# Performance work log

Hardware: AMD Instinct MI355X
Metric: run time of the kernel (lower is better)

## Reference

```python
import jax, jax.numpy as jnp
import numpy as np
from jax import lax

REPR, ACT, HID = 256, 2, 512
BN_EPS = 1e-5


def setup_inputs() -> dict:
    key = jax.random.key(0)
    ks = jax.random.split(key, 12)
    B, H, W, Tm1 = 512, 64, 64, 16
    d_in = REPR + ACT
    s = lambda k, shape, scale: jax.random.normal(k, shape, dtype=jnp.float32) * scale
    return {
        "init_state": jax.random.normal(ks[0], (B, 2, H, W), dtype=jnp.float32),
        "actions": jax.random.normal(ks[1], (B, Tm1, ACT), dtype=jnp.float32),
        "conv_w": s(ks[2], (16, 2, 3, 3), (1.0 / np.sqrt(2 * 9))),
        "bn_gamma": jnp.ones((16,), jnp.float32),
        "bn_beta": jnp.zeros((16,), jnp.float32),
        "enc_fc_w": s(ks[3], (REPR, 16), (1.0 / np.sqrt(16))),
        "enc_fc_b": s(ks[4], (REPR,), 0.01),
        "gru_w_ih": s(ks[5], (3 * HID, d_in), (1.0 / np.sqrt(HID))),
        "gru_w_hh": s(ks[6], (3 * HID, HID), (1.0 / np.sqrt(HID))),
        "gru_b_ih": s(ks[7], (3 * HID,), (1.0 / np.sqrt(HID))),
        "gru_b_hh": s(ks[8], (3 * HID,), (1.0 / np.sqrt(HID))),
        "pred_fc_w": s(ks[9], (REPR, HID), (1.0 / np.sqrt(HID))),
        "pred_fc_b": s(ks[10], (REPR,), 0.01),
    }


def _encoder(x, conv_w, bn_gamma, bn_beta, enc_fc_w, enc_fc_b):
    # Conv2d(2->16, 3x3, stride 1, pad 1, no bias), NCHW
    y = lax.conv_general_dilated(x, conv_w, (1, 1), "SAME",
                                 dimension_numbers=("NCHW", "OIHW", "NCHW"))
    # BatchNorm2d in training mode: batch statistics over (N, H, W)
    mean = jnp.mean(y, axis=(0, 2, 3), keepdims=True)
    var = jnp.var(y, axis=(0, 2, 3), keepdims=True)
    y = (y - mean) * lax.rsqrt(var + BN_EPS)
    y = y * bn_gamma[None, :, None, None] + bn_beta[None, :, None, None]
    y = jax.nn.relu(y)
    # MaxPool2d(2, 2)
    y = lax.reduce_window(y, -jnp.inf, lax.max, (1, 1, 2, 2), (1, 1, 2, 2), "VALID")
    # AdaptiveAvgPool2d((1,1)) + flatten
    y = jnp.mean(y, axis=(2, 3))  # (B, 16)
    return y @ enc_fc_w.T + enc_fc_b  # (B, repr_dim)


def reference(init_state, actions, conv_w, bn_gamma, bn_beta, enc_fc_w, enc_fc_b,
              gru_w_ih, gru_w_hh, gru_b_ih, gru_b_hh, pred_fc_w, pred_fc_b):
    B = init_state.shape[0]
    s0 = _encoder(init_state, conv_w, bn_gamma, bn_beta, enc_fc_w, enc_fc_b)  # (B, R)

    def step(carry, u_t):
        s_prev, h = carry
        x = jnp.concatenate([s_prev, u_t], axis=-1)          # (B, R+A)
        gx = x @ gru_w_ih.T + gru_b_ih                        # (B, 3H)
        gh = h @ gru_w_hh.T + gru_b_hh                        # (B, 3H)
        gx_r, gx_z, gx_n = jnp.split(gx, 3, axis=-1)
        gh_r, gh_z, gh_n = jnp.split(gh, 3, axis=-1)
        r = jax.nn.sigmoid(gx_r + gh_r)
        z = jax.nn.sigmoid(gx_z + gh_z)
        n = jnp.tanh(gx_n + r * gh_n)
        h_new = (1.0 - z) * n + z * h
        s_pred = jax.nn.relu(h_new @ pred_fc_w.T + pred_fc_b)  # (B, R)
        return (s_pred, h_new), s_pred

    h0 = jnp.zeros((B, HID), dtype=s0.dtype)
    u_seq = jnp.transpose(actions, (1, 0, 2))  # (T-1, B, A)
    _, preds = lax.scan(step, (s0, h0), u_seq)  # preds: (T-1, B, R)
    pred_encs = jnp.concatenate([s0[None], preds], axis=0)  # (T, B, R)
    return jnp.transpose(pred_encs, (1, 0, 2))  # (B, T, R)
```

## Files before the change

kernel.cpp:

```cpp
#include <hip/hip_runtime.h>
#include <hip/hip_bf16.h>
#include <math.h>

#define TM1 16
#define TT 17

typedef __attribute__((ext_vector_type(8))) __bf16 bf16x8;
typedef __attribute__((ext_vector_type(4))) float f32x4;

#define OFF_BSTATS 0
#define OFF_STATS  65536
#define OFF_POOLED 65568
#define OFF_BCOL   98336
#define OFF_SPB    104480
#define OFF_PWB    170016
#define OFF_WIHB   235552
#define OFF_WHHB   432160
#define OFF_HB     825376
#define OFF_RP     1087520

#define IMG_STRIDE 67
#define SLAB_ROWS 18
#define IMG_CI (SLAB_ROWS * IMG_STRIDE)

__device__ __forceinline__ void stage_slab_bf16(__hip_bfloat16* __restrict__ imgp,
                                                const float* __restrict__ xb, int slab,
                                                int tid) {
  for (int i = tid; i < 2 * SLAB_ROWS * 66; i += 256) {
    const int ci = i / (SLAB_ROWS * 66);
    const int rem = i - ci * (SLAB_ROWS * 66);
    const int lr = rem / 66, c = rem - lr * 66;
    const int gr = slab * 16 - 1 + lr;
    float v = 0.0f;
    if (gr >= 0 && gr < 64 && c >= 1 && c <= 64) v = xb[ci * 4096 + gr * 64 + (c - 1)];
    imgp[ci * IMG_CI + lr * IMG_STRIDE + c] = __float2bfloat16(v);
  }
}

__device__ __forceinline__ void make_k_offsets(int hi, int* off, int* val) {
#pragma unroll
  for (int j = 0; j < 8; ++j) {
    const int k = hi * 8 + j;
    if (k < 18) {
      const int ci = k / 9, r9 = k - ci * 9;
      const int dy = r9 / 3, dx = r9 - dy * 3;
      off[j] = ci * IMG_CI + dy * IMG_STRIDE + dx;
      val[j] = 1;
    } else {
      off[j] = 0;
      val[j] = 0;
    }
  }
}

__device__ __forceinline__ bf16x8 make_conv_bfrag(const float* __restrict__ cw,
                                                  int l15, int hi) {
  __hip_bfloat16 btmp[8];
#pragma unroll
  for (int j = 0; j < 8; ++j) {
    const int k = hi * 8 + j;
    btmp[j] = __float2bfloat16((k < 18) ? cw[l15 * 18 + k] : 0.0f);
  }
  return *(bf16x8*)btmp;
}

__device__ __forceinline__ bf16x8 make_conv_afrag(const __hip_bfloat16* __restrict__ imgp,
                                                  int yloc, int x0, int l15,
                                                  const int* off, const int* val) {
  const int base = yloc * IMG_STRIDE + x0 + l15;
  const __hip_bfloat16 z = __float2bfloat16(0.0f);
  __hip_bfloat16 atmp[8];
#pragma unroll
  for (int j = 0; j < 8; ++j) atmp[j] = val[j] ? imgp[base + off[j]] : z;
  return *(bf16x8*)atmp;
}

__global__ __launch_bounds__(256) void enc_stats_prep(
    const float* __restrict__ x, const float* __restrict__ cw,
    float* __restrict__ bstats,
    const float* __restrict__ wih, const float* __restrict__ whh,
    const float* __restrict__ pw,
    const float* __restrict__ bih, const float* __restrict__ bhh,
    __hip_bfloat16* __restrict__ wihb, __hip_bfloat16* __restrict__ whhb,
    __hip_bfloat16* __restrict__ pwb, float* __restrict__ bcol) {
  {
    const int n1 = 1536 * 256, n2 = 1536 * 512, n3 = 256 * 512, n4 = 512 * 12;
    int i = blockIdx.x * 256 + threadIdx.x;
    int st = gridDim.x * 256;
    for (int j = i; j < n1 + n2 + n3 + n4; j += st) {
      if (j < n1) {
        int r = j >> 8, c = j & 255;
        wihb[j] = __float2bfloat16(wih[r * 258 + c]);
      } else if (j < n1 + n2) {
        int k = j - n1;
        whhb[k] = __float2bfloat16(whh[k]);
      } else if (j < n1 + n2 + n3) {
        int k = j - n1 - n2;
        pwb[k] = __float2bfloat16(pw[k]);
      } else {
        int k = j - n1 - n2 - n3;
        int col = k / 12, e = k - col * 12;
        float v = 0.0f;
        switch (e) {
          case 0: v = bih[col] + bhh[col]; break;
          case 1: v = bih[512 + col] + bhh[512 + col]; break;
          case 2: v = bih[1024 + col]; break;
          case 3: v = bhh[1024 + col]; break;
          case 4: v = wih[col * 258 + 256]; break;
          case 5: v = wih[col * 258 + 257]; break;
          case 6: v = wih[(512 + col) * 258 + 256]; break;
          case 7: v = wih[(512 + col) * 258 + 257]; break;
          case 8: v = wih[(1024 + col) * 258 + 256]; break;
          case 9: v = wih[(1024 + col) * 258 + 257]; break;
          default: v = 0.0f; break;
        }
        bcol[k] = v;
      }
    }
  }

  __shared__ __hip_bfloat16 imgp[2 * IMG_CI];
  __shared__ float redS[4][16], redQ[4][16];
  const int tid = threadIdx.x;
  const int b = blockIdx.x >> 2, slab = blockIdx.x & 3;
  const int wv = tid >> 6, lane = tid & 63;
  const int l15 = lane & 15, hi = lane >> 4;
  stage_slab_bf16(imgp, x + b * 8192, slab, tid);

  int off[8], val[8];
  make_k_offsets(hi, off, val);
  const bf16x8 bfrag = make_conv_bfrag(cw, l15, hi);
  __syncthreads();

  float sacc = 0.0f, qacc = 0.0f;
  const f32x4 zero4 = {0.f, 0.f, 0.f, 0.f};
#pragma unroll
  for (int tp = 0; tp < 8; ++tp) {
    const int tpi = wv * 8 + tp;
    const int y0 = (tpi >> 2) * 2, x0 = (tpi & 3) * 16;
    bf16x8 a0 = make_conv_afrag(imgp, y0, x0, l15, off, val);
    bf16x8 a1 = make_conv_afrag(imgp, y0 + 1, x0, l15, off, val);
    f32x4 c0 = __builtin_amdgcn_mfma_f32_16x16x32_bf16(a0, bfrag, zero4, 0, 0, 0);
    f32x4 c1 = __builtin_amdgcn_mfma_f32_16x16x32_bf16(a1, bfrag, zero4, 0, 0, 0);
#pragma unroll
    for (int i = 0; i < 4; ++i) {
      sacc += c0[i] + c1[i];
      qacc = fmaf(c0[i], c0[i], qacc);
      qacc = fmaf(c1[i], c1[i], qacc);
    }
  }
  sacc += __shfl_down(sacc, 16); sacc += __shfl_down(sacc, 32);
  qacc += __shfl_down(qacc, 16); qacc += __shfl_down(qacc, 32);
  if (lane < 16) { redS[wv][l15] = sacc; redQ[wv][l15] = qacc; }
  __syncthreads();
  if (tid < 16)
    bstats[tid * 2048 + blockIdx.x] =
        redS[0][tid] + redS[1][tid] + redS[2][tid] + redS[3][tid];
  else if (tid < 32) {
    int c = tid - 16;
    bstats[tid * 2048 + blockIdx.x] =
        redQ[0][c] + redQ[1][c] + redQ[2][c] + redQ[3][c];
  }
}

__global__ __launch_bounds__(256) void reduce_stats_k(const float* __restrict__ bstats,
                                                      float* __restrict__ stats) {
  __shared__ float acc[4];
  const int c = blockIdx.x, tid = threadIdx.x;
  const float4 v4 = *(const float4*)(bstats + c * 2048 + tid * 8);
  const float4 w4 = *(const float4*)(bstats + c * 2048 + tid * 8 + 4);
  float v = v4.x + v4.y + v4.z + v4.w + w4.x + w4.y + w4.z + w4.w;
#pragma unroll
  for (int off = 32; off >= 1; off >>= 1) v += __shfl_down(v, off);
  if ((tid & 63) == 0) acc[tid >> 6] = v;
  __syncthreads();
  if (tid == 0) stats[c] = acc[0] + acc[1] + acc[2] + acc[3];
}

__global__ __launch_bounds__(256) void enc_pool(const float* __restrict__ x,
                                                const float* __restrict__ cw,
                                                const float* __restrict__ stats,
                                                const float* __restrict__ gamma,
                                                const float* __restrict__ beta,
                                                float* __restrict__ pooledG) {
  __shared__ __hip_bfloat16 imgp[2 * IMG_CI];
  __shared__ float red[4][16];
  __shared__ float statsL[32];
  const int tid = threadIdx.x;
  const int b = blockIdx.x >> 2, slab = blockIdx.x & 3;
  const int wv = tid >> 6, lane = tid & 63;
  const int l15 = lane & 15, hi = lane >> 4;
  stage_slab_bf16(imgp, x + b * 8192, slab, tid);
  if (tid < 32) statsL[tid] = stats[tid];

  int off[8], val[8];
  make_k_offsets(hi, off, val);
  const bf16x8 bfrag = make_conv_bfrag(cw, l15, hi);
  __syncthreads();

  const float invN = 1.0f / (512.0f * 4096.0f);
  const float m = statsL[l15] * invN;
  const float var = statsL[16 + l15] * invN - m * m;
  const float isd = rsqrtf(var + 1e-5f);
  const float scv = gamma[l15] * isd;
  const float shv = beta[l15] - m * scv;

  float psum = 0.0f;
  const f32x4 zero4 = {0.f, 0.f, 0.f, 0.f};
#pragma unroll
  for (int tp = 0; tp < 8; ++tp) {
    const int tpi = wv * 8 + tp;
    const int y0 = (tpi >> 2) * 2, x0 = (tpi & 3) * 16;
    bf16x8 a0 = make_conv_afrag(imgp, y0, x0, l15, off, val);
    bf16x8 a1 = make_conv_afrag(imgp, y0 + 1, x0, l15, off, val);
    f32x4 c0 = __builtin_amdgcn_mfma_f32_16x16x32_bf16(a0, bfrag, zero4, 0, 0, 0);
    f32x4 c1 = __builtin_amdgcn_mfma_f32_16x16x32_bf16(a1, bfrag, zero4, 0, 0, 0);
#pragma unroll
    for (int p = 0; p < 2; ++p) {
      const float v00 = fmaxf(fmaf(c0[2 * p + 0], scv, shv), 0.0f);
      const float v01 = fmaxf(fmaf(c0[2 * p + 1], scv, shv), 0.0f);
      const float v10 = fmaxf(fmaf(c1[2 * p + 0], scv, shv), 0.0f);
      const float v11 = fmaxf(fmaf(c1[2 * p + 1], scv, shv), 0.0f);
      psum += fmaxf(fmaxf(v00, v01), fmaxf(v10, v11));
    }
  }
  psum += __shfl_down(psum, 16);
  psum += __shfl_down(psum, 32);
  if (lane < 16) red[wv][l15] = psum;
  __syncthreads();
  if (tid < 16)
    pooledG[blockIdx.x * 16 + tid] = red[0][tid] + red[1][tid] + red[2][tid] + red[3][tid];
}

__global__ __launch_bounds__(384) void gru_v3(
    const __hip_bfloat16* __restrict__ hb_in,
    __hip_bfloat16* __restrict__ hb_out,
    const float* __restrict__ rp_in,
    float* __restrict__ rp_out,
    const __hip_bfloat16* __restrict__ wihb,
    const __hip_bfloat16* __restrict__ whhb,
    const __hip_bfloat16* __restrict__ pwb,
    const float* __restrict__ pb,
    const float* __restrict__ bcol,
    const float* __restrict__ actions,
    const float* __restrict__ pooledG, const float* __restrict__ fcw,
    const float* __restrict__ fcb,
    float* __restrict__ out,
    int t) {
  __shared__ __hip_bfloat16 hF[16 * 64 * 8];
  __shared__ __hip_bfloat16 sL[8 * 64 * 8];
  __shared__ __hip_bfloat16 hS[2 * 64 * 8];
  __shared__ float accL[4][4][256];
  const int tid = threadIdx.x;
  const int w = tid / 64, lane = tid & 63;
  const int l15 = lane & 15, hi = lane >> 4;
  const int cg = blockIdx.x >> 5, band = blockIdx.x & 31;
  const int row0 = band * 16;

  if (t > 0) {
    for (int i = tid; i < 1024; i += 384) {
      int kk = i >> 6, ln = i & 63;
      *(bf16x8*)(hF + i * 8) =
          *(const bf16x8*)(hb_in + (row0 + (ln & 15)) * 512 + kk * 32 + (ln >> 4) * 8);
    }
    for (int i = tid; i < 1024; i += 384) {
      const int row = i >> 6, c4 = (i & 63) * 4;
      float4 a = *(const float4*)(pb + c4);
#pragma unroll
      for (int s = 0; s < 8; ++s) {
        const float4 p = *(const float4*)(rp_in + ((size_t)(s * 512 + row0 + row)) * 256 + c4);
        a.x += p.x; a.y += p.y; a.z += p.z; a.w += p.w;
      }
      a.x = fmaxf(a.x, 0.f); a.y = fmaxf(a.y, 0.f);
      a.z = fmaxf(a.z, 0.f); a.w = fmaxf(a.w, 0.f);
      const float av[4] = {a.x, a.y, a.z, a.w};
#pragma unroll
      for (int j = 0; j < 4; ++j) {
        const int c = c4 + j;
        sL[((c >> 5) * 64 + row + 16 * ((c & 31) >> 3)) * 8 + (c & 7)] =
            __float2bfloat16(av[j]);
      }
      if (cg == 0) *(float4*)(out + ((size_t)(row0 + row) * TT + t) * 256 + c4) = a;
    }
  } else {
    float* avgF = &accL[0][0][0];
    if (tid < 256) {
      const int r = tid >> 4, k = tid & 15;
      const int img = row0 + r;
      const float v = pooledG[(img * 4 + 0) * 16 + k] + pooledG[(img * 4 + 1) * 16 + k] +
                      pooledG[(img * 4 + 2) * 16 + k] + pooledG[(img * 4 + 3) * 16 + k];
      avgF[r * 16 + k] = v * (1.0f / 1024.0f);
    }
    __syncthreads();
    for (int i = tid; i < 4096; i += 384) {
      const int r = i >> 8, col = i & 255;
      float v = fcb[col];
#pragma unroll
      for (int k = 0; k < 16; ++k) v = fmaf(avgF[r * 16 + k], fcw[col * 16 + k], v);
      sL[((col >> 5) * 64 + r + 16 * ((col & 31) >> 3)) * 8 + (col & 7)] =
          __float2bfloat16(v);
      if (cg == 0) out[((size_t)(row0 + r) * TT + 0) * 256 + col] = v;
    }
  }
  __syncthreads();

#pragma unroll
  for (int jj = 0; jj < 2; ++jj) {
    const int job = 2 * w + jj;
    const int g = job >> 2, ct4 = job & 3;
    const int jb = cg * 64 + ct4 * 16 + l15;
    f32x4 accS = {0.f, 0.f, 0.f, 0.f}, accH = accS;
    {
      const __hip_bfloat16* B = wihb + (size_t)(g * 512 + jb) * 256 + hi * 8;
#pragma unroll
      for (int kk = 0; kk < 8; ++kk) {
        bf16x8 a = *(const bf16x8*)(sL + (kk * 64 + lane) * 8);
        accS = __builtin_amdgcn_mfma_f32_16x16x32_bf16(a, *(const bf16x8*)(B + kk * 32),
                                                       accS, 0, 0, 0);
      }
    }
    if (t > 0) {
      const __hip_bfloat16* B = whhb + (size_t)(g * 512 + jb) * 512 + hi * 8;
#pragma unroll
      for (int kk = 0; kk < 16; ++kk) {
        bf16x8 a = *(const bf16x8*)(hF + (kk * 64 + lane) * 8);
        accH = __builtin_amdgcn_mfma_f32_16x16x32_bf16(a, *(const bf16x8*)(B + kk * 32),
                                                       accH, 0, 0, 0);
      }
    }
    if (g < 2) {
#pragma unroll
      for (int i = 0; i < 4; ++i)
        accL[g][ct4][(hi * 4 + i) * 16 + l15] = accS[i] + accH[i];
    } else {
#pragma unroll
      for (int i = 0; i < 4; ++i) {
        accL[2][ct4][(hi * 4 + i) * 16 + l15] = accS[i];
        accL[3][ct4][(hi * 4 + i) * 16 + l15] = accH[i];
      }
    }
  }
  __syncthreads();

  if (w < 4) {
    f32x4 vR = *(const f32x4*)&accL[0][w][lane * 4];
    f32x4 vZ = *(const f32x4*)&accL[1][w][lane * 4];
    f32x4 vXN = *(const f32x4*)&accL[2][w][lane * 4];
    f32x4 vHN = *(const f32x4*)&accL[3][w][lane * 4];
    const int r = lane >> 2;
    const int row = row0 + r;
    const float u0 = actions[row * 32 + t * 2 + 0];
    const float u1 = actions[row * 32 + t * 2 + 1];
#pragma unroll
    for (int j = 0; j < 4; ++j) {
      const int c = (lane & 3) * 4 + j;
      const int kloc = w * 16 + c;
      const int col = cg * 64 + kloc;
      const float4 b0 = *(const float4*)(bcol + col * 12);
      const float4 b1 = *(const float4*)(bcol + col * 12 + 4);
      const float4 b2 = *(const float4*)(bcol + col * 12 + 8);
      const float gr = vR[j] + b0.x + u0 * b1.x + u1 * b1.y;
      const float gz = vZ[j] + b0.y + u0 * b1.z + u1 * b1.w;
      const float gxn = vXN[j] + b0.z + u0 * b2.x + u1 * b2.y;
      const float ghn = vHN[j] + b0.w;
      const float rg = 1.0f / (1.0f + __expf(-gr));
      const float zg = 1.0f / (1.0f + __expf(-gz));
      float xn = gxn + rg * ghn;
      xn = fminf(fmaxf(xn, -15.0f), 15.0f);
      const float e = __expf(2.0f * xn);
      const float ng = (e - 1.0f) / (e + 1.0f);
      const float hp = (t > 0) ? (float)hb_in[row * 512 + col] : 0.0f;
      const float hnv = (1.0f - zg) * ng + zg * hp;
      const __hip_bfloat16 hb = __float2bfloat16(hnv);
      hb_out[row * 512 + col] = hb;
      hS[((kloc >> 5) * 64 + r + 16 * ((kloc & 31) >> 3)) * 8 + (kloc & 7)] = hb;
    }
  }
  __syncthreads();

  if (t < TM1 - 1) {
    for (int ct = w; ct < 16; ct += 6) {
      const int pc = ct * 16 + l15;
      const __hip_bfloat16* bp = pwb + (size_t)pc * 512 + cg * 64 + hi * 8;
      f32x4 acc = {0.f, 0.f, 0.f, 0.f};
      acc = __builtin_amdgcn_mfma_f32_16x16x32_bf16(
          *(const bf16x8*)(hS + (0 * 64 + lane) * 8), *(const bf16x8*)(bp), acc, 0, 0, 0);
      acc = __builtin_amdgcn_mfma_f32_16x16x32_bf16(
          *(const bf16x8*)(hS + (1 * 64 + lane) * 8), *(const bf16x8*)(bp + 32), acc, 0, 0, 0);
#pragma unroll
      for (int i = 0; i < 4; ++i)
        rp_out[((size_t)(cg * 512 + row0 + hi * 4 + i)) * 256 + pc] = acc[i];
    }
  }
}

__global__ __launch_bounds__(256) void pred_v2(
    const __hip_bfloat16* __restrict__ hb,
    const __hip_bfloat16* __restrict__ pwb,
    const float* __restrict__ pb,
    float* __restrict__ out,
    __hip_bfloat16* __restrict__ spb,
    int slot) {
  __shared__ float accL[4][256];
  const int tid = threadIdx.x;
  const int w = tid >> 6, lane = tid & 63;
  const int l15 = lane & 15, hi = lane >> 4;
  const int pcg = blockIdx.x, band = blockIdx.y;
  const int row0 = band * 16, pc0 = pcg * 16;
  f32x4 acc = {0.f, 0.f, 0.f, 0.f};
  const __hip_bfloat16* A = hb + (row0 + l15) * 512 + w * 128 + hi * 8;
  const __hip_bfloat16* B = pwb + (pc0 + l15) * 512 + w * 128 + hi * 8;
#pragma unroll
  for (int kk = 0; kk < 4; ++kk)
    acc = __builtin_amdgcn_mfma_f32_16x16x32_bf16(*(const bf16x8*)(A + kk * 32),
                                                  *(const bf16x8*)(B + kk * 32),
                                                  acc, 0, 0, 0);
#pragma unroll
  for (int i = 0; i < 4; ++i) accL[w][(hi * 4 + i) * 16 + l15] = acc[i];
  __syncthreads();
  if (w == 0) {
    f32x4 p0 = *(const f32x4*)&accL[0][lane * 4];
    f32x4 p1 = *(const f32x4*)&accL[1][lane * 4];
    f32x4 p2 = *(const f32x4*)&accL[2][lane * 4];
    f32x4 p3 = *(const f32x4*)&accL[3][lane * 4];
    const int r = lane >> 2;
    const int row = row0 + r;
    float4 ov;
    float* po = &ov.x;
#pragma unroll
    for (int j = 0; j < 4; ++j) {
      const int c = (lane & 3) * 4 + j;
      const int col = pc0 + c;
      float v = p0[j] + p1[j] + p2[j] + p3[j] + pb[col];
      v = fmaxf(v, 0.0f);
      po[j] = v;
      spb[row * 256 + col] = __float2bfloat16(v);
    }
    *(float4*)(out + ((size_t)row * TT + slot) * 256 + pc0 + (lane & 3) * 4) = ov;
  }
}

extern "C" void kernel_launch(void* const* d_in, const int* in_sizes, int n_in,
                              void* d_out, int out_size, void* d_ws, size_t ws_size,
                              hipStream_t stream) {
  const float* x       = (const float*)d_in[0];
  const float* actions = (const float*)d_in[1];
  const float* cw      = (const float*)d_in[2];
  const float* gamma   = (const float*)d_in[3];
  const float* beta    = (const float*)d_in[4];
  const float* fcw     = (const float*)d_in[5];
  const float* fcb     = (const float*)d_in[6];
  const float* wih     = (const float*)d_in[7];
  const float* whh     = (const float*)d_in[8];
  const float* bih     = (const float*)d_in[9];
  const float* bhh     = (const float*)d_in[10];
  const float* pw      = (const float*)d_in[11];
  const float* pb      = (const float*)d_in[12];
  float* out = (float*)d_out;
  float* ws  = (float*)d_ws;

  float* bstats  = ws + OFF_BSTATS;
  float* stats   = ws + OFF_STATS;
  float* pooledG = ws + OFF_POOLED;
  float* bcol    = ws + OFF_BCOL;
  __hip_bfloat16* spb  = (__hip_bfloat16*)(ws + OFF_SPB);
  __hip_bfloat16* pwb  = (__hip_bfloat16*)(ws + OFF_PWB);
  __hip_bfloat16* wihb = (__hip_bfloat16*)(ws + OFF_WIHB);
  __hip_bfloat16* whhb = (__hip_bfloat16*)(ws + OFF_WHHB);
  __hip_bfloat16* hb0  = (__hip_bfloat16*)(ws + OFF_HB);
  __hip_bfloat16* hb1  = hb0 + 512 * 512;
  float* rp0 = ws + OFF_RP;
  float* rp1 = rp0 + 8 * 512 * 256;

  enc_stats_prep<<<dim3(2048), dim3(256), 0, stream>>>(x, cw, bstats, wih, whh, pw,
                                                       bih, bhh, wihb, whhb, pwb, bcol);
  reduce_stats_k<<<dim3(32), dim3(256), 0, stream>>>(bstats, stats);
  enc_pool<<<dim3(2048), dim3(256), 0, stream>>>(x, cw, stats, gamma, beta, pooledG);
  for (int t = 0; t < TM1; ++t) {
    __hip_bfloat16* hbi = (t & 1) ? hb1 : hb0;
    __hip_bfloat16* hbo = (t & 1) ? hb0 : hb1;
    float* rpi = (t & 1) ? rp1 : rp0;
    float* rpo = (t & 1) ? rp0 : rp1;
    gru_v3<<<dim3(256), dim3(384), 0, stream>>>(
        hbi, hbo, rpi, rpo, wihb, whhb, pwb, pb, bcol, actions,
        pooledG, fcw, fcb, out, t);
  }
  pred_v2<<<dim3(16, 32), dim3(256), 0, stream>>>(hb0, pwb, pb, out, spb, 16);
}
```

Before: 306.5 us.

## Split GRU step over 512 blocks with bf16 prediction partials and direct h loads

The per-step GRU kernel now covers 32 hidden columns per block instead of 64, so the grid doubles to 512 blocks and each wave handles a single gate/column job. The partial prediction sums move from fp32 to bf16 and split across 16 column groups, which halves the bytes per partial but doubles how many are summed. The recurrent h operand is read straight from global memory rather than staged in shared memory, removing a staging loop and shrinking LDS use. Risks are lower precision from bf16 partial sums and more redundant reads of the input-side activation and weights across the extra blocks.

New measurement: 414.4 us. +35.2%, slower.

```diff
diff --git a/kernel.cpp b/kernel.cpp
--- a/kernel.cpp
+++ b/kernel.cpp
@@ -6,6 +6,7 @@
 #define TT 17
 
 typedef __attribute__((ext_vector_type(8))) __bf16 bf16x8;
+typedef __attribute__((ext_vector_type(4))) __bf16 bf16x4;
 typedef __attribute__((ext_vector_type(4))) float f32x4;
 
 #define OFF_BSTATS 0
@@ -232,11 +233,11 @@
     pooledG[blockIdx.x * 16 + tid] = red[0][tid] + red[1][tid] + red[2][tid] + red[3][tid];
 }
 
-__global__ __launch_bounds__(384) void gru_v3(
+__global__ __launch_bounds__(384) void gru_v5(
     const __hip_bfloat16* __restrict__ hb_in,
     __hip_bfloat16* __restrict__ hb_out,
-    const float* __restrict__ rp_in,
-    float* __restrict__ rp_out,
+    const __hip_bfloat16* __restrict__ rp_in,
+    __hip_bfloat16* __restrict__ rp_out,
     const __hip_bfloat16* __restrict__ wihb,
     const __hip_bfloat16* __restrict__ whhb,
     const __hip_bfloat16* __restrict__ pwb,
@@ -247,10 +248,9 @@
     const float* __restrict__ fcb,
     float* __restrict__ out,
     int t) {
-  __shared__ __hip_bfloat16 hF[16 * 64 * 8];
   __shared__ __hip_bfloat16 sL[8 * 64 * 8];
-  __shared__ __hip_bfloat16 hS[2 * 64 * 8];
-  __shared__ float accL[4][4][256];
+  __shared__ __hip_bfloat16 hS[64 * 8];
+  __shared__ float accL[4][2][256];
   const int tid = threadIdx.x;
   const int w = tid / 64, lane = tid & 63;
   const int l15 = lane & 15, hi = lane >> 4;
@@ -259,28 +259,29 @@
 
   if (t > 0) {
     for (int i = tid; i < 1024; i += 384) {
-      int kk = i >> 6, ln = i & 63;
-      *(bf16x8*)(hF + i * 8) =
-          *(const bf16x8*)(hb_in + (row0 + (ln & 15)) * 512 + kk * 32 + (ln >> 4) * 8);
-    }
-    for (int i = tid; i < 1024; i += 384) {
       const int row = i >> 6, c4 = (i & 63) * 4;
-      float4 a = *(const float4*)(pb + c4);
-#pragma unroll
-      for (int s = 0; s < 8; ++s) {
-        const float4 p = *(const float4*)(rp_in + ((size_t)(s * 512 + row0 + row)) * 256 + c4);
-        a.x += p.x; a.y += p.y; a.z += p.z; a.w += p.w;
-      }
-      a.x = fmaxf(a.x, 0.f); a.y = fmaxf(a.y, 0.f);
-      a.z = fmaxf(a.z, 0.f); a.w = fmaxf(a.w, 0.f);
-      const float av[4] = {a.x, a.y, a.z, a.w};
+      float a[4];
+      {
+        const float4 pb4 = *(const float4*)(pb + c4);
+        a[0] = pb4.x; a[1] = pb4.y; a[2] = pb4.z; a[3] = pb4.w;
+      }
+#pragma unroll
+      for (int s = 0; s < 16; ++s) {
+        const bf16x4 p = *(const bf16x4*)(rp_in + ((size_t)(s * 512 + row0 + row)) * 256 + c4);
+#pragma unroll
+        for (int j = 0; j < 4; ++j) a[j] += (float)p[j];
+      }
+      float4 ov;
+      ov.x = fmaxf(a[0], 0.f); ov.y = fmaxf(a[1], 0.f);
+      ov.z = fmaxf(a[2], 0.f); ov.w = fmaxf(a[3], 0.f);
+      const float av[4] = {ov.x, ov.y, ov.z, ov.w};
 #pragma unroll
       for (int j = 0; j < 4; ++j) {
         const int c = c4 + j;
         sL[((c >> 5) * 64 + row + 16 * ((c & 31) >> 3)) * 8 + (c & 7)] =
             __float2bfloat16(av[j]);
       }
-      if (cg == 0) *(float4*)(out + ((size_t)(row0 + row) * TT + t) * 256 + c4) = a;
+      if (cg == 0) *(float4*)(out + ((size_t)(row0 + row) * TT + t) * 256 + c4) = ov;
     }
   } else {
     float* avgF = &accL[0][0][0];
@@ -301,14 +302,13 @@
           __float2bfloat16(v);
       if (cg == 0) out[((size_t)(row0 + r) * TT + 0) * 256 + col] = v;
     }
-  }
-  __syncthreads();
-
-#pragma unroll
-  for (int jj = 0; jj < 2; ++jj) {
-    const int job = 2 * w + jj;
-    const int g = job >> 2, ct4 = job & 3;
-    const int jb = cg * 64 + ct4 * 16 + l15;
+    __syncthreads();
+  }
+  __syncthreads();
+
+  {
+    const int g = w >> 1, ct2 = w & 1;
+    const int jb = cg * 32 + ct2 * 16 + l15;
     f32x4 accS = {0.f, 0.f, 0.f, 0.f}, accH = accS;
     {
       const __hip_bfloat16* B = wihb + (size_t)(g * 512 + jb) * 256 + hi * 8;
@@ -320,10 +320,11 @@
       }
     }
     if (t > 0) {
+      const __hip_bfloat16* A = hb_in + (row0 + l15) * 512 + hi * 8;
       const __hip_bfloat16* B = whhb + (size_t)(g * 512 + jb) * 512 + hi * 8;
 #pragma unroll
       for (int kk = 0; kk < 16; ++kk) {
-        bf16x8 a = *(const bf16x8*)(hF + (kk * 64 + lane) * 8);
+        bf16x8 a = *(const bf16x8*)(A + kk * 32);
         accH = __builtin_amdgcn_mfma_f32_16x16x32_bf16(a, *(const bf16x8*)(B + kk * 32),
                                                        accH, 0, 0, 0);
       }
@@ -331,18 +332,18 @@
     if (g < 2) {
 #pragma unroll
       for (int i = 0; i < 4; ++i)
-        accL[g][ct4][(hi * 4 + i) * 16 + l15] = accS[i] + accH[i];
+        accL[g][ct2][(hi * 4 + i) * 16 + l15] = accS[i] + accH[i];
     } else {
 #pragma unroll
       for (int i = 0; i < 4; ++i) {
-        accL[2][ct4][(hi * 4 + i) * 16 + l15] = accS[i];
-        accL[3][ct4][(hi * 4 + i) * 16 + l15] = accH[i];
-      }
-    }
-  }
-  __syncthreads();
-
-  if (w < 4) {
+        accL[2][ct2][(hi * 4 + i) * 16 + l15] = accS[i];
+        accL[3][ct2][(hi * 4 + i) * 16 + l15] = accH[i];
+      }
+    }
+  }
+  __syncthreads();
+
+  if (w < 2) {
     f32x4 vR = *(const f32x4*)&accL[0][w][lane * 4];
     f32x4 vZ = *(const f32x4*)&accL[1][w][lane * 4];
     f32x4 vXN = *(const f32x4*)&accL[2][w][lane * 4];
@@ -355,7 +356,7 @@
     for (int j = 0; j < 4; ++j) {
       const int c = (lane & 3) * 4 + j;
       const int kloc = w * 16 + c;
-      const int col = cg * 64 + kloc;
+      const int col = cg * 32 + kloc;
       const float4 b0 = *(const float4*)(bcol + col * 12);
       const float4 b1 = *(const float4*)(bcol + col * 12 + 4);
       const float4 b2 = *(const float4*)(bcol + col * 12 + 8);
@@ -373,23 +374,22 @@
       const float hnv = (1.0f - zg) * ng + zg * hp;
       const __hip_bfloat16 hb = __float2bfloat16(hnv);
       hb_out[row * 512 + col] = hb;
-      hS[((kloc >> 5) * 64 + r + 16 * ((kloc & 31) >> 3)) * 8 + (kloc & 7)] = hb;
+      hS[(r + 16 * (kloc >> 3)) * 8 + (kloc & 7)] = hb;
     }
   }
   __syncthreads();
 
   if (t < TM1 - 1) {
+    const bf16x8 afrag = *(const bf16x8*)(hS + lane * 8);
     for (int ct = w; ct < 16; ct += 6) {
       const int pc = ct * 16 + l15;
-      const __hip_bfloat16* bp = pwb + (size_t)pc * 512 + cg * 64 + hi * 8;
+      const __hip_bfloat16* bp = pwb + (size_t)pc * 512 + cg * 32 + hi * 8;
       f32x4 acc = {0.f, 0.f, 0.f, 0.f};
-      acc = __builtin_amdgcn_mfma_f32_16x16x32_bf16(
-          *(const bf16x8*)(hS + (0 * 64 + lane) * 8), *(const bf16x8*)(bp), acc, 0, 0, 0);
-      acc = __builtin_amdgcn_mfma_f32_16x16x32_bf16(
-          *(const bf16x8*)(hS + (1 * 64 + lane) * 8), *(const bf16x8*)(bp + 32), acc, 0, 0, 0);
+      acc = __builtin_amdgcn_mfma_f32_16x16x32_bf16(afrag, *(const bf16x8*)bp, acc, 0, 0, 0);
 #pragma unroll
       for (int i = 0; i < 4; ++i)
-        rp_out[((size_t)(cg * 512 + row0 + hi * 4 + i)) * 256 + pc] = acc[i];
+        rp_out[((size_t)(cg * 512 + row0 + hi * 4 + i)) * 256 + pc] =
+            __float2bfloat16(acc[i]);
     }
   }
 }
@@ -469,8 +469,8 @@
   __hip_bfloat16* whhb = (__hip_bfloat16*)(ws + OFF_WHHB);
   __hip_bfloat16* hb0  = (__hip_bfloat16*)(ws + OFF_HB);
   __hip_bfloat16* hb1  = hb0 + 512 * 512;
-  float* rp0 = ws + OFF_RP;
-  float* rp1 = rp0 + 8 * 512 * 256;
+  __hip_bfloat16* rp0  = (__hip_bfloat16*)(ws + OFF_RP);
+  __hip_bfloat16* rp1  = rp0 + 16 * 512 * 256;
 
   enc_stats_prep<<<dim3(2048), dim3(256), 0, stream>>>(x, cw, bstats, wih, whh, pw,
                                                        bih, bhh, wihb, whhb, pwb, bcol);
@@ -479,9 +479,9 @@
   for (int t = 0; t < TM1; ++t) {
     __hip_bfloat16* hbi = (t & 1) ? hb1 : hb0;
     __hip_bfloat16* hbo = (t & 1) ? hb0 : hb1;
-    float* rpi = (t & 1) ? rp1 : rp0;
-    float* rpo = (t & 1) ? rp0 : rp1;
-    gru_v3<<<dim3(256), dim3(384), 0, stream>>>(
+    __hip_bfloat16* rpi = (t & 1) ? rp1 : rp0;
+    __hip_bfloat16* rpo = (t & 1) ? rp0 : rp1;
+    gru_v5<<<dim3(512), dim3(384), 0, stream>>>(
         hbi, hbo, rpi, rpo, wihb, whhb, pwb, pb, bcol, actions,
         pooledG, fcw, fcb, out, t);
   }
```
